# Optimization experiments

Hardware: AMD Instinct MI355X
Metric: run time of the kernel (lower is better)

Reference implementation:

```python
import jax, jax.numpy as jnp
import numpy as np

B, H, W, T = 2, 48, 48, 48
DIM, NH, KS = 384, 6, 3
HD = DIM // NH
K3 = KS ** 3  # 27 local neighbors


def setup_inputs() -> dict:
    key = jax.random.key(0)
    k1, k2, k3 = jax.random.split(key, 3)
    q = jax.random.normal(k1, (B, H, W, T, DIM), dtype=jnp.float32)
    k = jax.random.normal(k2, (B, H, W, T, DIM), dtype=jnp.float32)
    rpb = jax.random.normal(k3, (NH, KS, KS, KS), dtype=jnp.float32) * 0.02
    # fixed displacement vectors: meshgrid of [-1, 0, 1]^3, 'ij' indexing -> (27, 3)
    vec = jnp.arange(-(KS // 2), KS // 2 + 1, dtype=jnp.float32)
    grid = jnp.stack(jnp.meshgrid(vec, vec, vec, indexing='ij'), axis=-1)
    v = grid.reshape(K3, 3)
    return {"q": q, "k": k, "rpb": rpb, "v": v}


def reference(q, k, rpb, v):
    scale = HD ** (-0.5)
    # (B,H,W,T,NH,HD), pre-scaled queries
    qh = q.reshape(B, H, W, T, NH, HD) * scale
    kh = k.reshape(B, H, W, T, NH, HD)
    pdr = KS // 2
    k_pad = jnp.pad(kh, ((0, 0), (pdr, pdr), (pdr, pdr), (pdr, pdr), (0, 0), (0, 0)))
    # local QK logits: for each of the 27 offsets, dot q with the shifted k.
    # Loop is over a fixed tiny neighborhood (27), not over data dims, and
    # avoids materializing a [27,B,H,W,T,C] gather tensor.
    logits = []
    for di in range(KS):
        for dj in range(KS):
            for dl in range(KS):
                ks = k_pad[:, di:di + H, dj:dj + W, dl:dl + T]  # (B,H,W,T,NH,HD)
                logits.append(jnp.einsum('bxyznd,bxyznd->bxyzn', qh, ks))
    attn = jnp.stack(logits, axis=-1)  # (B,H,W,T,NH,27)
    attn = attn + rpb.reshape(NH, K3)  # relative position bias
    attn = jax.nn.softmax(attn, axis=-1)
    # weighted sum of fixed displacement vectors: (B,H,W,T,NH,3)
    x = jnp.einsum('bxyzno,oc->bxyznc', attn, v)
    x = x.reshape(B, H, W, T, NH * 3)
    return x.transpose(0, 4, 1, 2, 3)  # (B, NH*3, H, W, T)
```

## Files before the change

kernel.cpp:

```cpp
#include <hip/hip_runtime.h>

namespace {

constexpr int DIM = 384;
constexpr int NH  = 6;
constexpr float L2E    = 1.44269504088896f;
constexpr float SCALE2 = 0.125f * L2E;

constexpr int TILES = 12 * 12 * 6;
constexpr int NBLK  = 2 * NH * TILES;
constexpr int NCOL  = 6 * 10 * 6;

typedef _Float16 half8  __attribute__((ext_vector_type(8)));
typedef _Float16 half2v __attribute__((ext_vector_type(2)));
typedef __fp16   fp16x2 __attribute__((ext_vector_type(2)));
typedef float    floatx4 __attribute__((ext_vector_type(4)));
typedef unsigned uintx4 __attribute__((ext_vector_type(4)));

__device__ __forceinline__ half2v pk(float a, float b) {
    fp16x2 t = __builtin_amdgcn_cvt_pkrtz(a, b);
    return __builtin_bit_cast(half2v, t);
}

__global__ __launch_bounds__(512, 2)
void natten_id(const float* __restrict__ q, const float* __restrict__ k,
               const float* __restrict__ rpb, float* __restrict__ out)
{
    __shared__ _Float16 k_lds[NCOL * 64];
    __shared__ unsigned tbl_lds[7 * 256];
    __shared__ float    rpbL[32];

    const int bid0 = blockIdx.x;
    const int bid  = (bid0 & 7) * (NBLK / 8) + (bid0 >> 3);
    const int n    = bid % NH;
    const int tile = (bid / NH) % TILES;
    const int b    = bid / (NH * TILES);
    const int tz = (tile % 6) * 8;
    const int ty = ((tile / 6) % 12) * 4;
    const int tx = (tile / 72) * 4;

    const int tid = threadIdx.x;
    const int w = tid >> 6, lane = tid & 63;
    const int lrow = lane & 15, lgrp = lane >> 4;
    char* kl = (char*)k_lds;

    if (tid < 32) rpbL[tid] = (tid < 27) ? rpb[n * 27 + tid] * L2E : -1e30f;

    #pragma unroll
    for (int i = 0; i < 4; ++i) {
        const int e = i * 512 + tid;
        if (e < 1792) {
            const int j = e >> 8;
            const int u = j * 16 + (((e >> 6) & 3) << 2) + (e & 3);
            const int lr = (e >> 2) & 15;
            unsigned val = 124u | 0x01010100u;
            if (u < 108) {
                const int rx = u / 36, rem = u - rx * 36;
                const int rz = rem / 6, ry = rem - rz * 6;
                const int dj = ry - (lr >> 2), dl = rz - (lr & 3);
                if ((unsigned)dj <= 2u && (unsigned)dl <= 2u)
                    val = (unsigned)(((rx * 9 + dj * 3 + dl) << 2)
                          | (rx << 8) | (dj << 16) | (dl << 24));
            }
            tbl_lds[e] = val;
        }
    }

    const float* kb = k + (size_t)b * 110592 * DIM + n * 64;
    {
        const int col0 = tid >> 3, ch = tid & 7;
        int cx = col0 / 60, rem = col0 - cx * 60;
        int cz = rem / 6, cy = rem - cz * 6;
        char* dst = kl + col0 * 128 + ((ch * 16) ^ ((col0 & 7) << 4));
        #pragma unroll
        for (int it = 0; it < 6; ++it) {
            if (col0 + it * 64 < NCOL) {
                const int gx = tx + cx - 1, gy = ty + cy - 1, gz = tz + cz - 1;
                const bool v = ((unsigned)gx < 48u) && ((unsigned)gy < 48u) &&
                               ((unsigned)gz < 48u);
                const int cgx = min(max(gx, 0), 47);
                const int cgy = min(max(gy, 0), 47);
                const int cgz = min(max(gz, 0), 47);
                const float* s = kb + ((cgx * 48 + cgy) * 48 + cgz) * DIM + ch * 8;
                const float4 f0 = ((const float4*)s)[0];
                const float4 f1 = ((const float4*)s)[1];
                const unsigned m = v ? 0xFFFFFFFFu : 0u;
                half8 h;
                ((half2v*)&h)[0] = pk(f0.x, f0.y);
                ((half2v*)&h)[1] = pk(f0.z, f0.w);
                ((half2v*)&h)[2] = pk(f1.x, f1.y);
                ((half2v*)&h)[3] = pk(f1.z, f1.w);
                uintx4 hv = __builtin_bit_cast(uintx4, h);
                const uintx4 m4 = {m, m, m, m};
                hv &= m4;
                *(uintx4*)(dst + it * 8192) = hv;
            }
            cy += 4; if (cy >= 6)  { cy -= 6;  cz += 1; }
            cx += 1; if (cz >= 10) { cz -= 10; cx += 1; }
        }
    }

    const int mx = w >> 1, mz = (w & 1) * 4;
    const int qy = lrow >> 2, qz = lrow & 3;
    half8 a0, a1;
    {
        const float* qp = q + ((size_t)b * 110592
            + (size_t)(((tx + mx) * 48 + (ty + qy)) * 48 + (tz + mz + qz))) * DIM
            + n * 64 + lgrp * 8;
        const float4 f0 = ((const float4*)qp)[0];
        const float4 f1 = ((const float4*)qp)[1];
        const float4 g0 = ((const float4*)(qp + 32))[0];
        const float4 g1 = ((const float4*)(qp + 32))[1];
        ((half2v*)&a0)[0] = pk(f0.x, f0.y); ((half2v*)&a0)[1] = pk(f0.z, f0.w);
        ((half2v*)&a0)[2] = pk(f1.x, f1.y); ((half2v*)&a0)[3] = pk(f1.z, f1.w);
        ((half2v*)&a1)[0] = pk(g0.x, g0.y); ((half2v*)&a1)[1] = pk(g0.z, g0.w);
        ((half2v*)&a1)[2] = pk(g1.x, g1.y); ((half2v*)&a1)[3] = pk(g1.z, g1.w);
    }
    __syncthreads();

    const int wbase = mx * 60 + mz * 6;
    floatx4 acc[7];
    #pragma unroll
    for (int j = 0; j < 7; ++j) {
        const int u  = j * 16 + lrow;
        const int rx = (u >= 36 ? 1 : 0) + (u >= 72 ? 1 : 0);
        const int c  = min(wbase + u + 24 * rx, NCOL - 1);
        const char* base = kl + c * 128;
        const unsigned xm = (unsigned)(c & 7) << 4;
        const half8 b0 = *(const half8*)(base + ((lgrp * 16) ^ xm));
        const half8 b1 = *(const half8*)(base + ((lgrp * 16 + 64) ^ xm));
        floatx4 cc = {0.f, 0.f, 0.f, 0.f};
        cc = __builtin_amdgcn_mfma_f32_16x16x32_f16(b0, a0, cc, 0, 0, 0);
        cc = __builtin_amdgcn_mfma_f32_16x16x32_f16(b1, a1, cc, 0, 0, 0);
        acc[j] = cc;
    }

    float den = 0.f, sx = 0.f, sy = 0.f, sz = 0.f;
    #pragma unroll
    for (int j = 0; j < 7; ++j) {
        const uintx4 tr = *(const uintx4*)&tbl_lds[j * 256 + lgrp * 64 + lrow * 4];
        #pragma unroll
        for (int r = 0; r < 4; ++r) {
            const unsigned t = tr[r];
            const float bias = *(const float*)((const char*)rpbL + (t & 124u));
            const float e = __builtin_amdgcn_exp2f(fmaf(acc[j][r], SCALE2, bias));
            den += e;
            sx = fmaf(e, (float)((t >> 8) & 255u), sx);
            sy = fmaf(e, (float)((t >> 16) & 255u), sy);
            sz = fmaf(e, (float)(t >> 24), sz);
        }
    }
    den += __shfl_xor(den, 16); den += __shfl_xor(den, 32);
    sx  += __shfl_xor(sx, 16);  sx  += __shfl_xor(sx, 32);
    sy  += __shfl_xor(sy, 16);  sy  += __shfl_xor(sy, 32);
    sz  += __shfl_xor(sz, 16);  sz  += __shfl_xor(sz, 32);

    if (lgrp < 3) {
        const float s = (lgrp == 0) ? sx : (lgrp == 1 ? sy : sz);
        const float res = s / den - 1.0f;
        out[((size_t)(b * 18 + n * 3 + lgrp) * 48 + (tx + mx)) * 2304
            + (size_t)(ty + qy) * 48 + (tz + mz + qz)] = res;
    }
}

}

extern "C" void kernel_launch(void* const* d_in, const int* in_sizes, int n_in,
                              void* d_out, int out_size, void* d_ws, size_t ws_size,
                              hipStream_t stream)
{
    (void)in_sizes; (void)n_in; (void)d_ws; (void)ws_size; (void)out_size;
    const float* q   = (const float*)d_in[0];
    const float* k   = (const float*)d_in[1];
    const float* rpb = (const float*)d_in[2];
    float* out = (float*)d_out;

    natten_id<<<dim3(NBLK), dim3(512), 0, stream>>>(q, k, rpb, out);
}
```

Before: 177.8 us.

## Enlarge query tile to 8x8x4 with 1024-thread blocks and compact lookup table

Each block now covers an 8x8x4 query tile with 16 wavefronts instead of a 4x4x8 tile with 8. The K halo staged in shared memory becomes 10x10x6 columns, so the redundant halo reload per query drops. The per-lane neighbor table is packed into one byte per entry, and displacement and bias values come from a small float4 lookup rather than bitfield decoding. The cost is higher LDS use per block and fewer blocks in the grid, which may lower occupancy and load balance.

```diff
diff --git a/kernel.cpp b/kernel.cpp
--- a/kernel.cpp
+++ b/kernel.cpp
@@ -7,9 +7,9 @@
 constexpr float L2E    = 1.44269504088896f;
 constexpr float SCALE2 = 0.125f * L2E;
 
-constexpr int TILES = 12 * 12 * 6;
+constexpr int TILES = 6 * 6 * 12;
 constexpr int NBLK  = 2 * NH * TILES;
-constexpr int NCOL  = 6 * 10 * 6;
+constexpr int NCOL  = 10 * 10 * 6;
 
 typedef _Float16 half8  __attribute__((ext_vector_type(8)));
 typedef _Float16 half2v __attribute__((ext_vector_type(2)));
@@ -22,59 +22,69 @@
     return __builtin_bit_cast(half2v, t);
 }
 
-__global__ __launch_bounds__(512, 2)
-void natten_id(const float* __restrict__ q, const float* __restrict__ k,
-               const float* __restrict__ rpb, float* __restrict__ out)
+__global__ __launch_bounds__(1024, 8)
+void natten_w32(const float* __restrict__ q, const float* __restrict__ k,
+                const float* __restrict__ rpb, float* __restrict__ out)
 {
     __shared__ _Float16 k_lds[NCOL * 64];
-    __shared__ unsigned tbl_lds[7 * 256];
-    __shared__ float    rpbL[32];
+    __shared__ unsigned tbl_lds[7 * 64];
+    __shared__ float4   decoL[32];
 
     const int bid0 = blockIdx.x;
     const int bid  = (bid0 & 7) * (NBLK / 8) + (bid0 >> 3);
     const int n    = bid % NH;
     const int tile = (bid / NH) % TILES;
     const int b    = bid / (NH * TILES);
-    const int tz = (tile % 6) * 8;
-    const int ty = ((tile / 6) % 12) * 4;
-    const int tx = (tile / 72) * 4;
+    const int tz = (tile % 12) * 4;
+    const int ty = ((tile / 12) % 6) * 8;
+    const int tx = (tile / 72) * 8;
 
     const int tid = threadIdx.x;
     const int w = tid >> 6, lane = tid & 63;
     const int lrow = lane & 15, lgrp = lane >> 4;
     char* kl = (char*)k_lds;
 
-    if (tid < 32) rpbL[tid] = (tid < 27) ? rpb[n * 27 + tid] * L2E : -1e30f;
+    if (tid < 32) {
+        float4 d = make_float4(0.f, 0.f, 0.f, -1e30f);
+        if (tid < 27) {
+            const int rx = tid / 9, rem = tid - rx * 9;
+            const int dj = rem / 3, dl = rem - dj * 3;
+            d = make_float4((float)(rx - 1), (float)(dj - 1), (float)(dl - 1),
+                            rpb[n * 27 + tid] * L2E);
+        }
+        decoL[tid] = d;
+    }
 
-    #pragma unroll
-    for (int i = 0; i < 4; ++i) {
-        const int e = i * 512 + tid;
-        if (e < 1792) {
-            const int j = e >> 8;
-            const int u = j * 16 + (((e >> 6) & 3) << 2) + (e & 3);
-            const int lr = (e >> 2) & 15;
-            unsigned val = 124u | 0x01010100u;
+    if (tid < 448) {
+        const int j = tid >> 6, lane_e = tid & 63;
+        const int lgrp_e = lane_e >> 4, lrow_e = lane_e & 15;
+        const int qy = lrow_e >> 2, qz = lrow_e & 3;
+        unsigned word = 0;
+        #pragma unroll
+        for (int r = 0; r < 4; ++r) {
+            const int u = j * 16 + lgrp_e * 4 + r;
+            unsigned byte = 124u;
             if (u < 108) {
                 const int rx = u / 36, rem = u - rx * 36;
-                const int rz = rem / 6, ry = rem - rz * 6;
-                const int dj = ry - (lr >> 2), dl = rz - (lr & 3);
+                const int ry = rem / 6, rz = rem - ry * 6;
+                const int dj = ry - qy, dl = rz - qz;
                 if ((unsigned)dj <= 2u && (unsigned)dl <= 2u)
-                    val = (unsigned)(((rx * 9 + dj * 3 + dl) << 2)
-                          | (rx << 8) | (dj << 16) | (dl << 24));
+                    byte = (unsigned)((rx * 9 + dj * 3 + dl) * 4);
             }
-            tbl_lds[e] = val;
+            word |= byte << (r * 8);
         }
+        tbl_lds[tid] = word;
     }
 
     const float* kb = k + (size_t)b * 110592 * DIM + n * 64;
     {
         const int col0 = tid >> 3, ch = tid & 7;
         int cx = col0 / 60, rem = col0 - cx * 60;
-        int cz = rem / 6, cy = rem - cz * 6;
+        int cy = rem / 6, cz = rem - cy * 6;
         char* dst = kl + col0 * 128 + ((ch * 16) ^ ((col0 & 7) << 4));
         #pragma unroll
-        for (int it = 0; it < 6; ++it) {
-            if (col0 + it * 64 < NCOL) {
+        for (int it = 0; it < 5; ++it) {
+            if (it < 4 || col0 < NCOL - 512) {
                 const int gx = tx + cx - 1, gy = ty + cy - 1, gz = tz + cz - 1;
                 const bool v = ((unsigned)gx < 48u) && ((unsigned)gy < 48u) &&
                                ((unsigned)gz < 48u);
@@ -93,19 +103,20 @@
                 uintx4 hv = __builtin_bit_cast(uintx4, h);
                 const uintx4 m4 = {m, m, m, m};
                 hv &= m4;
-                *(uintx4*)(dst + it * 8192) = hv;
+                *(uintx4*)(dst + it * 16384) = hv;
             }
-            cy += 4; if (cy >= 6)  { cy -= 6;  cz += 1; }
-            cx += 1; if (cz >= 10) { cz -= 10; cx += 1; }
+            cz += 2; if (cz >= 6)  { cz -= 6;  cy += 1; }
+            cy += 1; if (cy >= 10) { cy -= 10; cx += 1; }
+            cx += 2;
         }
     }
 
-    const int mx = w >> 1, mz = (w & 1) * 4;
+    const int mx = w >> 1, my = (w & 1) * 4;
     const int qy = lrow >> 2, qz = lrow & 3;
     half8 a0, a1;
     {
         const float* qp = q + ((size_t)b * 110592
-            + (size_t)(((tx + mx) * 48 + (ty + qy)) * 48 + (tz + mz + qz))) * DIM
+            + (size_t)(((tx + mx) * 48 + (ty + my + qy)) * 48 + (tz + qz))) * DIM
             + n * 64 + lgrp * 8;
         const float4 f0 = ((const float4*)qp)[0];
         const float4 f1 = ((const float4*)qp)[1];
@@ -118,7 +129,7 @@
     }
     __syncthreads();
 
-    const int wbase = mx * 60 + mz * 6;
+    const int wbase = mx * 60 + my * 6;
     floatx4 acc[7];
     #pragma unroll
     for (int j = 0; j < 7; ++j) {
@@ -138,16 +149,16 @@
     float den = 0.f, sx = 0.f, sy = 0.f, sz = 0.f;
     #pragma unroll
     for (int j = 0; j < 7; ++j) {
-        const uintx4 tr = *(const uintx4*)&tbl_lds[j * 256 + lgrp * 64 + lrow * 4];
+        const unsigned word = tbl_lds[j * 64 + lane];
         #pragma unroll
         for (int r = 0; r < 4; ++r) {
-            const unsigned t = tr[r];
-            const float bias = *(const float*)((const char*)rpbL + (t & 124u));
-            const float e = __builtin_amdgcn_exp2f(fmaf(acc[j][r], SCALE2, bias));
+            const unsigned off = ((word >> (r * 8)) & 255u) << 2;
+            const float4 d = *(const float4*)((const char*)decoL + off);
+            const float e = __builtin_amdgcn_exp2f(fmaf(acc[j][r], SCALE2, d.w));
             den += e;
-            sx = fmaf(e, (float)((t >> 8) & 255u), sx);
-            sy = fmaf(e, (float)((t >> 16) & 255u), sy);
-            sz = fmaf(e, (float)(t >> 24), sz);
+            sx = fmaf(e, d.x, sx);
+            sy = fmaf(e, d.y, sy);
+            sz = fmaf(e, d.z, sz);
         }
     }
     den += __shfl_xor(den, 16); den += __shfl_xor(den, 32);
@@ -157,9 +168,8 @@
 
     if (lgrp < 3) {
         const float s = (lgrp == 0) ? sx : (lgrp == 1 ? sy : sz);
-        const float res = s / den - 1.0f;
         out[((size_t)(b * 18 + n * 3 + lgrp) * 48 + (tx + mx)) * 2304
-            + (size_t)(ty + qy) * 48 + (tz + mz + qz)] = res;
+            + (size_t)(ty + my + qy) * 48 + (tz + qz)] = s / den;
     }
 }
 
@@ -175,5 +185,5 @@
     const float* rpb = (const float*)d_in[2];
     float* out = (float*)d_out;
 
-    natten_id<<<dim3(NBLK), dim3(512), 0, stream>>>(q, k, rpb, out);
+    natten_w32<<<dim3(NBLK), dim3(1024), 0, stream>>>(q, k, rpb, out);
 }
```

New measurement: 216.5 us. 21.8% more time.

## Stage K tile in two channel halves with padded LDS stride to raise occupancy

Applied to the files above, without the earlier changes.

Splits the K-neighborhood staging into two passes over 32-channel halves. Each pass reuses a smaller LDS buffer with a padded row stride of 80 bytes in place of the XOR swizzle, and its MFMA accumulates into persistent accumulators. This cuts LDS per block roughly in half, and launch bounds are raised to 6 blocks per CU to allow more resident waves. The cost is two extra barriers and serialization between staging and compute within a block.

```diff
diff --git a/kernel.cpp b/kernel.cpp
--- a/kernel.cpp
+++ b/kernel.cpp
@@ -10,6 +10,7 @@
 constexpr int TILES = 12 * 12 * 6;
 constexpr int NBLK  = 2 * NH * TILES;
 constexpr int NCOL  = 6 * 10 * 6;
+constexpr int KSTR  = 80;
 
 typedef _Float16 half8  __attribute__((ext_vector_type(8)));
 typedef _Float16 half2v __attribute__((ext_vector_type(2)));
@@ -22,11 +23,11 @@
     return __builtin_bit_cast(half2v, t);
 }
 
-__global__ __launch_bounds__(512, 2)
-void natten_id(const float* __restrict__ q, const float* __restrict__ k,
+__global__ __launch_bounds__(512, 6)
+void natten_ks(const float* __restrict__ q, const float* __restrict__ k,
                const float* __restrict__ rpb, float* __restrict__ out)
 {
-    __shared__ _Float16 k_lds[NCOL * 64];
+    __shared__ _Float16 k_lds[NCOL * (KSTR / 2)];
     __shared__ unsigned tbl_lds[7 * 256];
     __shared__ float    rpbL[32];
 
@@ -67,38 +68,50 @@
     }
 
     const float* kb = k + (size_t)b * 110592 * DIM + n * 64;
+    const int ch4 = tid & 3;
+    int koff[3];
+    unsigned um[3];
     {
-        const int col0 = tid >> 3, ch = tid & 7;
+        const int col0 = tid >> 2;
         int cx = col0 / 60, rem = col0 - cx * 60;
         int cz = rem / 6, cy = rem - cz * 6;
-        char* dst = kl + col0 * 128 + ((ch * 16) ^ ((col0 & 7) << 4));
         #pragma unroll
-        for (int it = 0; it < 6; ++it) {
-            if (col0 + it * 64 < NCOL) {
-                const int gx = tx + cx - 1, gy = ty + cy - 1, gz = tz + cz - 1;
-                const bool v = ((unsigned)gx < 48u) && ((unsigned)gy < 48u) &&
-                               ((unsigned)gz < 48u);
-                const int cgx = min(max(gx, 0), 47);
-                const int cgy = min(max(gy, 0), 47);
-                const int cgz = min(max(gz, 0), 47);
-                const float* s = kb + ((cgx * 48 + cgy) * 48 + cgz) * DIM + ch * 8;
+        for (int i = 0; i < 3; ++i) {
+            const int gx = tx + cx - 1, gy = ty + cy - 1, gz = tz + cz - 1;
+            const bool v = ((unsigned)gx < 48u) && ((unsigned)gy < 48u) &&
+                           ((unsigned)gz < 48u);
+            const int cgx = min(max(gx, 0), 47);
+            const int cgy = min(max(gy, 0), 47);
+            const int cgz = min(max(gz, 0), 47);
+            koff[i] = ((cgx * 48 + cgy) * 48 + cgz) * DIM + ch4 * 8;
+            um[i] = v ? 0xFFFFFFFFu : 0u;
+            cy += 2; if (cy >= 6)  { cy -= 6;  cz += 1; }
+            cz += 1; if (cz >= 10) { cz -= 10; cx += 1; }
+            cx += 2;
+        }
+    }
+    const int dst0 = (tid >> 2) * KSTR + ch4 * 16;
+
+    auto stage = [&](int p) {
+        #pragma unroll
+        for (int i = 0; i < 3; ++i) {
+            const int u = tid + i * 512;
+            if (u < NCOL * 4) {
+                const float* s = kb + koff[i] + p * 32;
                 const float4 f0 = ((const float4*)s)[0];
                 const float4 f1 = ((const float4*)s)[1];
-                const unsigned m = v ? 0xFFFFFFFFu : 0u;
                 half8 h;
                 ((half2v*)&h)[0] = pk(f0.x, f0.y);
                 ((half2v*)&h)[1] = pk(f0.z, f0.w);
                 ((half2v*)&h)[2] = pk(f1.x, f1.y);
                 ((half2v*)&h)[3] = pk(f1.z, f1.w);
                 uintx4 hv = __builtin_bit_cast(uintx4, h);
-                const uintx4 m4 = {m, m, m, m};
+                const uintx4 m4 = {um[i], um[i], um[i], um[i]};
                 hv &= m4;
-                *(uintx4*)(dst + it * 8192) = hv;
+                *(uintx4*)(kl + dst0 + i * 128 * KSTR) = hv;
             }
-            cy += 4; if (cy >= 6)  { cy -= 6;  cz += 1; }
-            cx += 1; if (cz >= 10) { cz -= 10; cx += 1; }
         }
-    }
+    };
 
     const int mx = w >> 1, mz = (w & 1) * 4;
     const int qy = lrow >> 2, qz = lrow & 3;
@@ -116,24 +129,27 @@
         ((half2v*)&a1)[0] = pk(g0.x, g0.y); ((half2v*)&a1)[1] = pk(g0.z, g0.w);
         ((half2v*)&a1)[2] = pk(g1.x, g1.y); ((half2v*)&a1)[3] = pk(g1.z, g1.w);
     }
-    __syncthreads();
 
     const int wbase = mx * 60 + mz * 6;
-    floatx4 acc[7];
-    #pragma unroll
-    for (int j = 0; j < 7; ++j) {
-        const int u  = j * 16 + lrow;
-        const int rx = (u >= 36 ? 1 : 0) + (u >= 72 ? 1 : 0);
-        const int c  = min(wbase + u + 24 * rx, NCOL - 1);
-        const char* base = kl + c * 128;
-        const unsigned xm = (unsigned)(c & 7) << 4;
-        const half8 b0 = *(const half8*)(base + ((lgrp * 16) ^ xm));
-        const half8 b1 = *(const half8*)(base + ((lgrp * 16 + 64) ^ xm));
-        floatx4 cc = {0.f, 0.f, 0.f, 0.f};
-        cc = __builtin_amdgcn_mfma_f32_16x16x32_f16(b0, a0, cc, 0, 0, 0);
-        cc = __builtin_amdgcn_mfma_f32_16x16x32_f16(b1, a1, cc, 0, 0, 0);
-        acc[j] = cc;
-    }
+    floatx4 acc[7] = {};
+    auto pass = [&](half8 af) {
+        #pragma unroll
+        for (int j = 0; j < 7; ++j) {
+            const int u  = j * 16 + lrow;
+            const int rx = (u >= 36 ? 1 : 0) + (u >= 72 ? 1 : 0);
+            const int c  = min(wbase + u + 24 * rx, NCOL - 1);
+            const half8 bf = *(const half8*)(kl + c * KSTR + lgrp * 16);
+            acc[j] = __builtin_amdgcn_mfma_f32_16x16x32_f16(bf, af, acc[j], 0, 0, 0);
+        }
+    };
+
+    stage(0);
+    __syncthreads();
+    pass(a0);
+    __syncthreads();
+    stage(1);
+    __syncthreads();
+    pass(a1);
 
     float den = 0.f, sx = 0.f, sy = 0.f, sz = 0.f;
     #pragma unroll
@@ -175,5 +191,5 @@
     const float* rpb = (const float*)d_in[2];
     float* out = (float*)d_out;
 
-    natten_id<<<dim3(NBLK), dim3(512), 0, stream>>>(q, k, rpb, out);
+    natten_ks<<<dim3(NBLK), dim3(512), 0, stream>>>(q, k, rpb, out);
 }
```

After: 194.2 us. 9.2% more time.
